# Kernel optimization log

Hardware: AMD Instinct MI355X
Metric: run time of the kernel (lower is better)

Reference implementation:

```python
import jax, jax.numpy as jnp
import numpy as np

EMBED_DIM = 768
NUM_HEADS = 12
HEAD_DIM = EMBED_DIM // NUM_HEADS
SCALE = HEAD_DIM ** -0.5


def setup_inputs() -> dict:
    key = jax.random.key(0)
    ks = jax.random.split(key, 5)
    B, N, D = 2, 4096, EMBED_DIM
    std = 1.0 / np.sqrt(D)
    x = jax.random.normal(ks[0], (B, N, D), dtype=jnp.float32)
    W_qkv = jax.random.normal(ks[1], (D, 3 * D), dtype=jnp.float32) * std
    b_qkv = jax.random.normal(ks[2], (3 * D,), dtype=jnp.float32) * 0.01
    W_proj = jax.random.normal(ks[3], (D, D), dtype=jnp.float32) * std
    b_proj = jax.random.normal(ks[4], (D,), dtype=jnp.float32) * 0.01
    return {"x": x, "W_qkv": W_qkv, "b_qkv": b_qkv, "W_proj": W_proj, "b_proj": b_proj}


def reference(x, W_qkv, b_qkv, W_proj, b_proj):
    B, N, D = x.shape
    H, Hd = NUM_HEADS, HEAD_DIM
    qkv = x @ W_qkv + b_qkv                      # [B, N, 3D]
    qkv = qkv.reshape(B, N, 3, H, Hd)
    qkv = jnp.transpose(qkv, (2, 0, 3, 1, 4))    # [3, B, H, N, Hd]
    q, k, v = qkv[0], qkv[1], qkv[2]
    attn = jnp.einsum('bhqd,bhkd->bhqk', q, k) * SCALE   # [B, H, N, N]
    attn = jax.nn.softmax(attn, axis=-1)
    out = jnp.einsum('bhqk,bhkd->bhqd', attn, v)          # [B, H, N, Hd]
    out = jnp.transpose(out, (0, 2, 1, 3)).reshape(B, N, D)
    return out @ W_proj + b_proj
```

## Files before the change

kernel.cpp:

```cpp
#include <hip/hip_runtime.h>
#include <hip/hip_bf16.h>

typedef __attribute__((ext_vector_type(4))) float f32x4;
typedef __attribute__((ext_vector_type(16))) float f32x16;
typedef __attribute__((ext_vector_type(8))) short s16x8;
typedef __attribute__((ext_vector_type(4))) unsigned int u32x4;

#define MFMA16(a, b, c) __builtin_amdgcn_mfma_f32_16x16x32_bf16(a, b, c, 0, 0, 0)
#define MFMA32(a, b, c) __builtin_amdgcn_mfma_f32_32x32x16_bf16(a, b, c, 0, 0, 0)

__device__ __forceinline__ short f2bf(float f) {
  unsigned u = __builtin_bit_cast(unsigned, f);
  u += 0x7fffu + ((u >> 16) & 1u);
  return (short)(u >> 16);
}
__device__ __forceinline__ unsigned cvtpk(float lo, float hi) {
  unsigned r;
  asm("v_cvt_pk_bf16_f32 %0, %1, %2" : "=v"(r) : "v"(lo), "v"(hi));
  return r;
}
__device__ __forceinline__ float ex2(float x) {
  float r;
  asm("v_exp_f32 %0, %1" : "=v"(r) : "v"(x));
  return r;
}
__device__ __forceinline__ void vperm(const s16x8 a, const s16x8 b,
                                      s16x8& w0, s16x8& w1) {
#pragma unroll
  for (int e = 0; e < 4; ++e) {
    w0[e] = a[e];
    w0[4 + e] = b[e];
    w1[e] = a[4 + e];
    w1[4 + e] = b[4 + e];
  }
}
__device__ __forceinline__ void gl_lds16(const unsigned short* g, short* l) {
  __builtin_amdgcn_global_load_lds(
      (const __attribute__((address_space(1))) unsigned int*)g,
      (__attribute__((address_space(3))) unsigned int*)l, 16, 0, 0);
}

__global__ __launch_bounds__(256) void convert_x(
    const float* __restrict__ X, unsigned short* __restrict__ Xb) {
  const size_t i = ((size_t)blockIdx.x * 256 + threadIdx.x) * 8;
  f32x4 a = *(const f32x4*)(X + i);
  f32x4 b = *(const f32x4*)(X + i + 4);
  s16x8 o;
#pragma unroll
  for (int e = 0; e < 4; ++e) o[e] = f2bf(a[e]);
#pragma unroll
  for (int e = 0; e < 4; ++e) o[4 + e] = f2bf(b[e]);
  *(s16x8*)(Xb + i) = o;
}

__global__ __launch_bounds__(256) void tconv(
    const float* __restrict__ W, unsigned short* __restrict__ Wt,
    int K, int N) {
  __shared__ float T[64][65];
  const int k0 = blockIdx.x * 64, n0 = blockIdx.y * 64;
  const int t = threadIdx.x;
  const int tr = t >> 4, tc = (t & 15) * 4;
#pragma unroll
  for (int i = 0; i < 4; ++i) {
    f32x4 v = *(const f32x4*)&W[(size_t)(k0 + tr + i * 16) * N + n0 + tc];
#pragma unroll
    for (int e = 0; e < 4; ++e) T[tc + e][tr + i * 16] = v[e];
  }
  __syncthreads();
  const int nn = t >> 2, kk = (t & 3) * 16;
  s16x8 o0, o1;
#pragma unroll
  for (int j = 0; j < 8; ++j) o0[j] = f2bf(T[nn][kk + j]);
#pragma unroll
  for (int j = 0; j < 8; ++j) o1[j] = f2bf(T[nn][kk + 8 + j]);
  *(s16x8*)&Wt[(size_t)(n0 + nn) * K + k0 + kk] = o0;
  *(s16x8*)&Wt[(size_t)(n0 + nn) * K + k0 + kk + 8] = o1;
}

__global__ __launch_bounds__(256) void qkv_gemm(
    const unsigned short* __restrict__ Xb, const unsigned short* __restrict__ Wt,
    const float* __restrict__ bias, unsigned short* __restrict__ Qo,
    unsigned short* __restrict__ Ko, unsigned short* __restrict__ VTo) {
  __shared__ __align__(16) short As[128 * 32];
  __shared__ __align__(16) short Bs[128 * 32];
  const int m0 = blockIdx.x * 128, n0 = blockIdx.y * 128;
  const int tid = threadIdx.x, lane = tid & 63, wid = tid >> 6;
  const int wr = wid >> 1, wc = wid & 1;
  const int lr = lane & 15, s4 = lane >> 4;

  const int crow = lane >> 2;
  const int ccol = (lane & 3) ^ (crow & 3);
  const unsigned short* ga0 = Xb + (size_t)(m0 + wid * 32 + crow) * 768 + ccol * 8;
  const unsigned short* ga1 = ga0 + (size_t)16 * 768;
  const unsigned short* gb0 = Wt + (size_t)(n0 + wid * 32 + crow) * 768 + ccol * 8;
  const unsigned short* gb1 = gb0 + (size_t)16 * 768;
  short* lA0 = &As[(wid * 2) * 512];
  short* lA1 = &As[(wid * 2 + 1) * 512];
  short* lB0 = &Bs[(wid * 2) * 512];
  short* lB1 = &Bs[(wid * 2 + 1) * 512];

  f32x4 acc[4][4];
#pragma unroll
  for (int i = 0; i < 4; ++i)
#pragma unroll
    for (int j = 0; j < 4; ++j)
#pragma unroll
      for (int e = 0; e < 4; ++e) acc[i][j][e] = 0.f;

  for (int k0 = 0; k0 < 768; k0 += 32) {
    gl_lds16(ga0 + k0, lA0);
    gl_lds16(ga1 + k0, lA1);
    gl_lds16(gb0 + k0, lB0);
    gl_lds16(gb1 + k0, lB1);
    __syncthreads();
    s16x8 af[4], bfr[4];
#pragma unroll
    for (int mi = 0; mi < 4; ++mi) {
      const int row = wr * 64 + mi * 16 + lr;
      af[mi] = *(const s16x8*)&As[row * 32 + ((s4 ^ (row & 3)) << 3)];
    }
#pragma unroll
    for (int ni = 0; ni < 4; ++ni) {
      const int row = wc * 64 + ni * 16 + lr;
      bfr[ni] = *(const s16x8*)&Bs[row * 32 + ((s4 ^ (row & 3)) << 3)];
    }
#pragma unroll
    for (int mi = 0; mi < 4; ++mi)
#pragma unroll
      for (int ni = 0; ni < 4; ++ni)
        acc[mi][ni] = MFMA16(af[mi], bfr[ni], acc[mi][ni]);
    __syncthreads();
  }

  const float QSC = 0.18033688011f;
  const int rbase = m0 + wr * 64 + (lane >> 4) * 4;
#pragma unroll
  for (int ni = 0; ni < 4; ++ni) {
    const int cb = n0 + wc * 64 + ni * 16;
    const int which = cb / 768;
    const int rem = cb - which * 768;
    const int h = rem >> 6;
    const int d = (rem & 63) + lr;
    const float bi = bias[cb + lr];
#pragma unroll
    for (int mi = 0; mi < 4; ++mi) {
#pragma unroll
      for (int j = 0; j < 4; ++j) {
        const int row = rbase + mi * 16 + j;
        const int bb = row >> 12, t = row & 4095;
        const float v = acc[mi][ni][j] + bi;
        const size_t hb = (size_t)(bb * 12 + h);
        if (which == 0)
          Qo[(hb * 4096 + t) * 64 + d] = (unsigned short)f2bf(v * QSC);
        else if (which == 1)
          Ko[(hb * 4096 + t) * 64 + d] = (unsigned short)f2bf(v);
        else
          VTo[(hb * 64 + d) * 4096 + t] = (unsigned short)f2bf(v);
      }
    }
  }
}

#define LP 72
#define TSZ (64 * LP)

__global__ __launch_bounds__(256) void attn_fwd(
    const unsigned short* __restrict__ Qg, const unsigned short* __restrict__ Kg,
    const unsigned short* __restrict__ VTg, unsigned short* __restrict__ Aout) {
  __shared__ __align__(16) short smem[4 * TSZ];
  const int qt = blockIdx.x, bh = blockIdx.y;
  const unsigned short* Qh = Qg + (size_t)bh * 4096 * 64;
  const unsigned short* Kh = Kg + (size_t)bh * 4096 * 64;
  const unsigned short* Vh = VTg + (size_t)bh * 4096 * 64;
  const int tid = threadIdx.x, lane = tid & 63, wid = tid >> 6;
  const int l31 = lane & 31, hi = lane >> 5;
  const int qbase = qt * 128 + wid * 32;

  s16x8 qf[4];
#pragma unroll
  for (int db = 0; db < 4; ++db)
    qf[db] = *(const s16x8*)&Qh[(size_t)(qbase + l31) * 64 + db * 16 + hi * 8];

  s16x8 ones;
#pragma unroll
  for (int e = 0; e < 8; ++e) ones[e] = (short)0x3F80;

  f32x16 zf;
#pragma unroll
  for (int r = 0; r < 16; ++r) zf[r] = 0.f;
  f32x16 o0 = zf, o1 = zf, accl = zf;

  const int srow = tid >> 2, sp = tid & 3;
  const int sd0 = srow * LP + sp * 16;
  const int sd1 = sd0 + 8;
  const unsigned short* kga = Kh + srow * 64 + sp * 16;
  const unsigned short* vga = Vh + (size_t)srow * 4096 + sp * 16;

  s16x8 kr0 = *(const s16x8*)kga;
  s16x8 kr1 = *(const s16x8*)(kga + 8);
  s16x8 vr0 = *(const s16x8*)vga;
  s16x8 vr1 = *(const s16x8*)(vga + 8);
  {
    s16x8 w0, w1;
    vperm(vr0, vr1, w0, w1);
    *(s16x8*)&smem[sd0] = kr0;
    *(s16x8*)&smem[sd1] = kr1;
    *(s16x8*)&smem[2 * TSZ + sd0] = w0;
    *(s16x8*)&smem[2 * TSZ + sd1] = w1;
  }
  __syncthreads();

  int cur = 0;
  for (int t = 0; t < 64; ++t) {
    if (t < 63) {
      kr0 = *(const s16x8*)(kga + (size_t)(t + 1) * 4096);
      kr1 = *(const s16x8*)(kga + (size_t)(t + 1) * 4096 + 8);
      vr0 = *(const s16x8*)(vga + (t + 1) * 64);
      vr1 = *(const s16x8*)(vga + (t + 1) * 64 + 8);
    }
    const short* Kc = smem + cur * TSZ;
    const short* Vc = smem + 2 * TSZ + cur * TSZ;

    f32x16 sA = zf, sB = zf;
    __builtin_amdgcn_s_setprio(1);
#pragma unroll
    for (int db = 0; db < 4; ++db) {
      s16x8 kf = *(const s16x8*)&Kc[l31 * LP + (db * 2 + hi) * 8];
      sA = MFMA32(kf, qf[db], sA);
    }
#pragma unroll
    for (int db = 0; db < 4; ++db) {
      s16x8 kf = *(const s16x8*)&Kc[(32 + l31) * LP + (db * 2 + hi) * 8];
      sB = MFMA32(kf, qf[db], sB);
    }
    __builtin_amdgcn_s_setprio(0);

#pragma unroll
    for (int r = 0; r < 16; ++r) {
      sA[r] = ex2(sA[r]);
      sB[r] = ex2(sB[r]);
    }
    s16x8 pf0, pf1, pf2, pf3;
#define PACK_PF(pfv, sv, bse)                                           \
  {                                                                     \
    u32x4 fw;                                                           \
    fw[0] = cvtpk(sv[bse + 0], sv[bse + 1]);                            \
    fw[1] = cvtpk(sv[bse + 2], sv[bse + 3]);                            \
    fw[2] = cvtpk(sv[bse + 4], sv[bse + 5]);                            \
    fw[3] = cvtpk(sv[bse + 6], sv[bse + 7]);                            \
    pfv = __builtin_bit_cast(s16x8, fw);                                \
  }
    PACK_PF(pf0, sA, 0)
    PACK_PF(pf1, sA, 8)
    PACK_PF(pf2, sB, 0)
    PACK_PF(pf3, sB, 8)
#undef PACK_PF

    __builtin_amdgcn_s_setprio(1);
    accl = MFMA32(ones, pf0, accl);
    accl = MFMA32(ones, pf1, accl);
    accl = MFMA32(ones, pf2, accl);
    accl = MFMA32(ones, pf3, accl);

    {
      const short* Vr = &Vc[l31 * LP];
      s16x8 v0 = *(const s16x8*)&Vr[(0 + hi) * 8];
      o0 = MFMA32(v0, pf0, o0);
      s16x8 v1 = *(const s16x8*)&Vr[(2 + hi) * 8];
      o0 = MFMA32(v1, pf1, o0);
      s16x8 v2 = *(const s16x8*)&Vr[(4 + hi) * 8];
      o0 = MFMA32(v2, pf2, o0);
      s16x8 v3 = *(const s16x8*)&Vr[(6 + hi) * 8];
      o0 = MFMA32(v3, pf3, o0);
      const short* Vr1 = &Vc[(32 + l31) * LP];
      s16x8 w0 = *(const s16x8*)&Vr1[(0 + hi) * 8];
      o1 = MFMA32(w0, pf0, o1);
      s16x8 w1 = *(const s16x8*)&Vr1[(2 + hi) * 8];
      o1 = MFMA32(w1, pf1, o1);
      s16x8 w2 = *(const s16x8*)&Vr1[(4 + hi) * 8];
      o1 = MFMA32(w2, pf2, o1);
      s16x8 w3 = *(const s16x8*)&Vr1[(6 + hi) * 8];
      o1 = MFMA32(w3, pf3, o1);
    }
    __builtin_amdgcn_s_setprio(0);

    if (t < 63) {
      const int nb = cur ^ 1;
      s16x8 w0, w1;
      vperm(vr0, vr1, w0, w1);
      *(s16x8*)&smem[nb * TSZ + sd0] = kr0;
      *(s16x8*)&smem[nb * TSZ + sd1] = kr1;
      *(s16x8*)&smem[2 * TSZ + nb * TSZ + sd0] = w0;
      *(s16x8*)&smem[2 * TSZ + nb * TSZ + sd1] = w1;
      __syncthreads();
      cur = nb;
    }
  }

  __syncthreads();
  short* Ow = smem + wid * (32 * 72);
  const float inv = 1.0f / accl[0];
#pragma unroll
  for (int r = 0; r < 16; ++r) {
    const int dd = (r & 3) + 8 * (r >> 2) + 4 * hi;
    Ow[l31 * 72 + dd] = f2bf(o0[r] * inv);
    Ow[l31 * 72 + 32 + dd] = f2bf(o1[r] * inv);
  }
  const int b = bh / 12, h = bh - b * 12;
  const int qq = lane >> 1, c0 = (lane & 1) * 32;
  const size_t gb = ((size_t)(b * 4096 + qbase + qq)) * 768 + h * 64 + c0;
#pragma unroll
  for (int i = 0; i < 4; ++i) {
    s16x8 v = *(const s16x8*)&Ow[qq * 72 + c0 + i * 8];
    *(s16x8*)&Aout[gb + i * 8] = v;
  }
}

__global__ __launch_bounds__(256) void proj_gemm(
    const unsigned short* __restrict__ A, const unsigned short* __restrict__ Wt,
    const float* __restrict__ bias, float* __restrict__ out) {
  __shared__ __align__(16) short As[128 * 32];
  __shared__ __align__(16) short Bs[128 * 32];
  const int m0 = blockIdx.x * 128, n0 = blockIdx.y * 128;
  const int tid = threadIdx.x, lane = tid & 63, wid = tid >> 6;
  const int wr = wid >> 1, wc = wid & 1;
  const int lr = lane & 15, s4 = lane >> 4;

  const int crow = lane >> 2;
  const int ccol = (lane & 3) ^ (crow & 3);
  const unsigned short* ga0 = A + (size_t)(m0 + wid * 32 + crow) * 768 + ccol * 8;
  const unsigned short* ga1 = ga0 + (size_t)16 * 768;
  const unsigned short* gb0 = Wt + (size_t)(n0 + wid * 32 + crow) * 768 + ccol * 8;
  const unsigned short* gb1 = gb0 + (size_t)16 * 768;
  short* lA0 = &As[(wid * 2) * 512];
  short* lA1 = &As[(wid * 2 + 1) * 512];
  short* lB0 = &Bs[(wid * 2) * 512];
  short* lB1 = &Bs[(wid * 2 + 1) * 512];

  f32x4 acc[4][4];
#pragma unroll
  for (int i = 0; i < 4; ++i)
#pragma unroll
    for (int j = 0; j < 4; ++j)
#pragma unroll
      for (int e = 0; e < 4; ++e) acc[i][j][e] = 0.f;

  for (int k0 = 0; k0 < 768; k0 += 32) {
    gl_lds16(ga0 + k0, lA0);
    gl_lds16(ga1 + k0, lA1);
    gl_lds16(gb0 + k0, lB0);
    gl_lds16(gb1 + k0, lB1);
    __syncthreads();
    s16x8 af[4], bfr[4];
#pragma unroll
    for (int mi = 0; mi < 4; ++mi) {
      const int row = wr * 64 + mi * 16 + lr;
      af[mi] = *(const s16x8*)&As[row * 32 + ((s4 ^ (row & 3)) << 3)];
    }
#pragma unroll
    for (int ni = 0; ni < 4; ++ni) {
      const int row = wc * 64 + ni * 16 + lr;
      bfr[ni] = *(const s16x8*)&Bs[row * 32 + ((s4 ^ (row & 3)) << 3)];
    }
#pragma unroll
    for (int mi = 0; mi < 4; ++mi)
#pragma unroll
      for (int ni = 0; ni < 4; ++ni)
        acc[mi][ni] = MFMA16(af[mi], bfr[ni], acc[mi][ni]);
    __syncthreads();
  }

  const int rbase = m0 + wr * 64 + (lane >> 4) * 4;
#pragma unroll
  for (int ni = 0; ni < 4; ++ni) {
    const int cb = n0 + wc * 64 + ni * 16;
    const float bi = bias[cb + lr];
#pragma unroll
    for (int mi = 0; mi < 4; ++mi) {
#pragma unroll
      for (int j = 0; j < 4; ++j) {
        const int row = rbase + mi * 16 + j;
        out[(size_t)row * 768 + cb + lr] = acc[mi][ni][j] + bi;
      }
    }
  }
}

extern "C" void kernel_launch(void* const* d_in, const int* in_sizes, int n_in,
                              void* d_out, int out_size, void* d_ws, size_t ws_size,
                              hipStream_t stream) {
  const float* x = (const float*)d_in[0];
  const float* W_qkv = (const float*)d_in[1];
  const float* b_qkv = (const float*)d_in[2];
  const float* W_proj = (const float*)d_in[3];
  const float* b_proj = (const float*)d_in[4];
  float* out = (float*)d_out;

  unsigned short* ws = (unsigned short*)d_ws;
  const size_t NQ = (size_t)24 * 4096 * 64;
  unsigned short* q = ws;
  unsigned short* k = ws + NQ;
  unsigned short* vt = ws + 2 * NQ;
  unsigned short* xb_attn = ws + 3 * NQ;
  unsigned short* wqt = ws + 4 * NQ;
  unsigned short* wpt = wqt + (size_t)2304 * 768;

  convert_x<<<3072, 256, 0, stream>>>(x, xb_attn);
  tconv<<<dim3(12, 36), 256, 0, stream>>>(W_qkv, wqt, 768, 2304);
  tconv<<<dim3(12, 12), 256, 0, stream>>>(W_proj, wpt, 768, 768);
  qkv_gemm<<<dim3(64, 18), 256, 0, stream>>>(xb_attn, wqt, b_qkv, q, k, vt);
  attn_fwd<<<dim3(32, 24), 256, 0, stream>>>(q, k, vt, xb_attn);
  proj_gemm<<<dim3(64, 6), 256, 0, stream>>>(xb_attn, wpt, b_proj, out);
}
```

Baseline: 232.5 us.

## Software-pipeline attention loop so PV of previous tile overlaps QK of current

Restructures the attention main loop so each iteration first does the P·V MFMAs for the previous key tile, then the QK MFMAs and exp/pack for the current tile. V tiles get a three-buffer rotation in LDS (LDS grows from 4 to 5 tiles) so the V tile still being read is not overwritten. The aim is to let the exp/convert VALU work interleave with independent MFMA work instead of sitting on the QK→softmax→PV dependency chain. The costs are extra LDS per block, which may lower occupancy, plus a prologue and epilogue.

Result: no change. 234.5 us (+0.9%).

```diff
diff --git a/kernel.cpp b/kernel.cpp
--- a/kernel.cpp
+++ b/kernel.cpp
@@ -167,7 +167,7 @@
 __global__ __launch_bounds__(256) void attn_fwd(
     const unsigned short* __restrict__ Qg, const unsigned short* __restrict__ Kg,
     const unsigned short* __restrict__ VTg, unsigned short* __restrict__ Aout) {
-  __shared__ __align__(16) short smem[4 * TSZ];
+  __shared__ __align__(16) short smem[5 * TSZ];
   const int qt = blockIdx.x, bh = blockIdx.y;
   const unsigned short* Qh = Qg + (size_t)bh * 4096 * 64;
   const unsigned short* Kh = Kg + (size_t)bh * 4096 * 64;
@@ -190,57 +190,34 @@
   for (int r = 0; r < 16; ++r) zf[r] = 0.f;
   f32x16 o0 = zf, o1 = zf, accl = zf;
 
+  short* const Kb0 = smem;
+  short* const Kb1 = smem + TSZ;
+  short* vrd = smem + 2 * TSZ;
+  short* vmd = smem + 3 * TSZ;
+  short* vwr = smem + 4 * TSZ;
+
   const int srow = tid >> 2, sp = tid & 3;
   const int sd0 = srow * LP + sp * 16;
   const int sd1 = sd0 + 8;
   const unsigned short* kga = Kh + srow * 64 + sp * 16;
   const unsigned short* vga = Vh + (size_t)srow * 4096 + sp * 16;
 
-  s16x8 kr0 = *(const s16x8*)kga;
-  s16x8 kr1 = *(const s16x8*)(kga + 8);
-  s16x8 vr0 = *(const s16x8*)vga;
-  s16x8 vr1 = *(const s16x8*)(vga + 8);
   {
+    s16x8 kr0 = *(const s16x8*)kga;
+    s16x8 kr1 = *(const s16x8*)(kga + 8);
+    s16x8 vr0 = *(const s16x8*)vga;
+    s16x8 vr1 = *(const s16x8*)(vga + 8);
     s16x8 w0, w1;
     vperm(vr0, vr1, w0, w1);
-    *(s16x8*)&smem[sd0] = kr0;
-    *(s16x8*)&smem[sd1] = kr1;
-    *(s16x8*)&smem[2 * TSZ + sd0] = w0;
-    *(s16x8*)&smem[2 * TSZ + sd1] = w1;
+    *(s16x8*)&Kb0[sd0] = kr0;
+    *(s16x8*)&Kb0[sd1] = kr1;
+    *(s16x8*)&vrd[sd0] = w0;
+    *(s16x8*)&vrd[sd1] = w1;
   }
   __syncthreads();
 
-  int cur = 0;
-  for (int t = 0; t < 64; ++t) {
-    if (t < 63) {
-      kr0 = *(const s16x8*)(kga + (size_t)(t + 1) * 4096);
-      kr1 = *(const s16x8*)(kga + (size_t)(t + 1) * 4096 + 8);
-      vr0 = *(const s16x8*)(vga + (t + 1) * 64);
-      vr1 = *(const s16x8*)(vga + (t + 1) * 64 + 8);
-    }
-    const short* Kc = smem + cur * TSZ;
-    const short* Vc = smem + 2 * TSZ + cur * TSZ;
-
-    f32x16 sA = zf, sB = zf;
-    __builtin_amdgcn_s_setprio(1);
-#pragma unroll
-    for (int db = 0; db < 4; ++db) {
-      s16x8 kf = *(const s16x8*)&Kc[l31 * LP + (db * 2 + hi) * 8];
-      sA = MFMA32(kf, qf[db], sA);
-    }
-#pragma unroll
-    for (int db = 0; db < 4; ++db) {
-      s16x8 kf = *(const s16x8*)&Kc[(32 + l31) * LP + (db * 2 + hi) * 8];
-      sB = MFMA32(kf, qf[db], sB);
-    }
-    __builtin_amdgcn_s_setprio(0);
-
-#pragma unroll
-    for (int r = 0; r < 16; ++r) {
-      sA[r] = ex2(sA[r]);
-      sB[r] = ex2(sB[r]);
-    }
-    s16x8 pf0, pf1, pf2, pf3;
+  s16x8 pf0, pf1, pf2, pf3;
+
 #define PACK_PF(pfv, sv, bse)                                           \
   {                                                                     \
     u32x4 fw;                                                           \
@@ -250,52 +227,115 @@
     fw[3] = cvtpk(sv[bse + 6], sv[bse + 7]);                            \
     pfv = __builtin_bit_cast(s16x8, fw);                                \
   }
-    PACK_PF(pf0, sA, 0)
-    PACK_PF(pf1, sA, 8)
-    PACK_PF(pf2, sB, 0)
-    PACK_PF(pf3, sB, 8)
-#undef PACK_PF
-
-    __builtin_amdgcn_s_setprio(1);
-    accl = MFMA32(ones, pf0, accl);
-    accl = MFMA32(ones, pf1, accl);
-    accl = MFMA32(ones, pf2, accl);
-    accl = MFMA32(ones, pf3, accl);
-
-    {
-      const short* Vr = &Vc[l31 * LP];
-      s16x8 v0 = *(const s16x8*)&Vr[(0 + hi) * 8];
-      o0 = MFMA32(v0, pf0, o0);
-      s16x8 v1 = *(const s16x8*)&Vr[(2 + hi) * 8];
-      o0 = MFMA32(v1, pf1, o0);
-      s16x8 v2 = *(const s16x8*)&Vr[(4 + hi) * 8];
-      o0 = MFMA32(v2, pf2, o0);
-      s16x8 v3 = *(const s16x8*)&Vr[(6 + hi) * 8];
-      o0 = MFMA32(v3, pf3, o0);
-      const short* Vr1 = &Vc[(32 + l31) * LP];
-      s16x8 w0 = *(const s16x8*)&Vr1[(0 + hi) * 8];
-      o1 = MFMA32(w0, pf0, o1);
-      s16x8 w1 = *(const s16x8*)&Vr1[(2 + hi) * 8];
-      o1 = MFMA32(w1, pf1, o1);
-      s16x8 w2 = *(const s16x8*)&Vr1[(4 + hi) * 8];
-      o1 = MFMA32(w2, pf2, o1);
-      s16x8 w3 = *(const s16x8*)&Vr1[(6 + hi) * 8];
-      o1 = MFMA32(w3, pf3, o1);
-    }
-    __builtin_amdgcn_s_setprio(0);
-
+
+#define QK_BLOCK(Kc, sA, sB)                                            \
+  {                                                                     \
+    __builtin_amdgcn_s_setprio(1);                                      \
+    _Pragma("unroll") for (int db = 0; db < 4; ++db) {                  \
+      s16x8 kf = *(const s16x8*)&(Kc)[l31 * LP + (db * 2 + hi) * 8];    \
+      sA = MFMA32(kf, qf[db], sA);                                      \
+    }                                                                   \
+    _Pragma("unroll") for (int db = 0; db < 4; ++db) {                  \
+      s16x8 kf = *(const s16x8*)&(Kc)[(32 + l31) * LP + (db * 2 + hi) * 8]; \
+      sB = MFMA32(kf, qf[db], sB);                                      \
+    }                                                                   \
+    __builtin_amdgcn_s_setprio(0);                                      \
+  }
+
+#define SOFTMAX_PACK(sA, sB)                                            \
+  {                                                                     \
+    _Pragma("unroll") for (int r = 0; r < 16; ++r) {                    \
+      sA[r] = ex2(sA[r]);                                               \
+      sB[r] = ex2(sB[r]);                                               \
+    }                                                                   \
+    PACK_PF(pf0, sA, 0)                                                 \
+    PACK_PF(pf1, sA, 8)                                                 \
+    PACK_PF(pf2, sB, 0)                                                 \
+    PACK_PF(pf3, sB, 8)                                                 \
+  }
+
+#define PV_BLOCK(Vc)                                                    \
+  {                                                                     \
+    __builtin_amdgcn_s_setprio(1);                                      \
+    accl = MFMA32(ones, pf0, accl);                                     \
+    accl = MFMA32(ones, pf1, accl);                                     \
+    accl = MFMA32(ones, pf2, accl);                                     \
+    accl = MFMA32(ones, pf3, accl);                                     \
+    const short* Vr = &(Vc)[l31 * LP];                                  \
+    s16x8 v0 = *(const s16x8*)&Vr[(0 + hi) * 8];                        \
+    o0 = MFMA32(v0, pf0, o0);                                           \
+    s16x8 v1 = *(const s16x8*)&Vr[(2 + hi) * 8];                        \
+    o0 = MFMA32(v1, pf1, o0);                                           \
+    s16x8 v2 = *(const s16x8*)&Vr[(4 + hi) * 8];                        \
+    o0 = MFMA32(v2, pf2, o0);                                           \
+    s16x8 v3 = *(const s16x8*)&Vr[(6 + hi) * 8];                        \
+    o0 = MFMA32(v3, pf3, o0);                                           \
+    const short* Vr1 = &(Vc)[(32 + l31) * LP];                          \
+    s16x8 w0 = *(const s16x8*)&Vr1[(0 + hi) * 8];                       \
+    o1 = MFMA32(w0, pf0, o1);                                           \
+    s16x8 w1 = *(const s16x8*)&Vr1[(2 + hi) * 8];                       \
+    o1 = MFMA32(w1, pf1, o1);                                           \
+    s16x8 w2 = *(const s16x8*)&Vr1[(4 + hi) * 8];                       \
+    o1 = MFMA32(w2, pf2, o1);                                           \
+    s16x8 w3 = *(const s16x8*)&Vr1[(6 + hi) * 8];                       \
+    o1 = MFMA32(w3, pf3, o1);                                           \
+    __builtin_amdgcn_s_setprio(0);                                      \
+  }
+
+  {
+    s16x8 kr0 = *(const s16x8*)(kga + (size_t)4096);
+    s16x8 kr1 = *(const s16x8*)(kga + (size_t)4096 + 8);
+    s16x8 vr0 = *(const s16x8*)(vga + 64);
+    s16x8 vr1 = *(const s16x8*)(vga + 64 + 8);
+    f32x16 sA = zf, sB = zf;
+    QK_BLOCK(Kb0, sA, sB)
+    SOFTMAX_PACK(sA, sB)
+    s16x8 w0, w1;
+    vperm(vr0, vr1, w0, w1);
+    *(s16x8*)&Kb1[sd0] = kr0;
+    *(s16x8*)&Kb1[sd1] = kr1;
+    *(s16x8*)&vmd[sd0] = w0;
+    *(s16x8*)&vmd[sd1] = w1;
+    __syncthreads();
+  }
+
+  for (int t = 1; t < 64; ++t) {
+    s16x8 kr0, kr1, vr0, vr1;
     if (t < 63) {
-      const int nb = cur ^ 1;
+      kr0 = *(const s16x8*)(kga + (size_t)(t + 1) * 4096);
+      kr1 = *(const s16x8*)(kga + (size_t)(t + 1) * 4096 + 8);
+      vr0 = *(const s16x8*)(vga + (t + 1) * 64);
+      vr1 = *(const s16x8*)(vga + (t + 1) * 64 + 8);
+    }
+    const short* Kc = (t & 1) ? Kb1 : Kb0;
+    short* Kw = (t & 1) ? Kb0 : Kb1;
+
+    PV_BLOCK(vrd)
+    f32x16 sA = zf, sB = zf;
+    QK_BLOCK(Kc, sA, sB)
+    SOFTMAX_PACK(sA, sB)
+
+    if (t < 63) {
       s16x8 w0, w1;
       vperm(vr0, vr1, w0, w1);
-      *(s16x8*)&smem[nb * TSZ + sd0] = kr0;
-      *(s16x8*)&smem[nb * TSZ + sd1] = kr1;
-      *(s16x8*)&smem[2 * TSZ + nb * TSZ + sd0] = w0;
-      *(s16x8*)&smem[2 * TSZ + nb * TSZ + sd1] = w1;
-      __syncthreads();
-      cur = nb;
-    }
-  }
+      *(s16x8*)&Kw[sd0] = kr0;
+      *(s16x8*)&Kw[sd1] = kr1;
+      *(s16x8*)&vwr[sd0] = w0;
+      *(s16x8*)&vwr[sd1] = w1;
+    }
+    __syncthreads();
+    short* tmp = vrd;
+    vrd = vmd;
+    vmd = vwr;
+    vwr = tmp;
+  }
+
+  PV_BLOCK(vrd)
+
+#undef PV_BLOCK
+#undef SOFTMAX_PACK
+#undef QK_BLOCK
+#undef PACK_PF
 
   __syncthreads();
   short* Ow = smem + wid * (32 * 72);
```
